# Kernel tuning notes

Hardware: AMD Instinct MI355X
Metric: run time of the kernel (lower is better)

## Reference

```python
import jax, jax.numpy as jnp
import numpy as np

IN_DIM, HID_DIM, OUT_DIM = 1024, 2048, 1024
DEG1, DEG2 = 8, 8
BATCH = 16384


def cheby_kan_layer(x, coeffs):
    """x: [b, i]; coeffs: [i, o, d+1] -> [b, o].
    Per-feature min-max normalize over batch to [-1,1], Chebyshev recurrence, contract."""
    degree = coeffs.shape[-1] - 1
    mn = jnp.min(x, axis=0, keepdims=True)
    mx = jnp.max(x, axis=0, keepdims=True)
    x = 2.0 * (x - mn) / (mx - mn) - 1.0
    Ts = [jnp.ones_like(x)]
    if degree > 0:
        Ts.append(x)
    for _ in range(2, degree + 1):
        Ts.append(2.0 * x * Ts[-1] - Ts[-2])
    cheby = jnp.stack(Ts, axis=-1)  # [b, i, d+1]
    return jnp.einsum('bid,iod->bo', cheby, coeffs)


def setup_inputs() -> dict:
    key = jax.random.key(0)
    k1, k2, k3 = jax.random.split(key, 3)
    x = jax.random.normal(k1, (BATCH, IN_DIM), dtype=jnp.float32)
    # kaiming-uniform-ish init for coeffs
    b1 = float(np.sqrt(6.0 / IN_DIM))
    b2 = float(np.sqrt(6.0 / HID_DIM))
    coeffs1 = jax.random.uniform(k2, (IN_DIM, HID_DIM, DEG1 + 1), dtype=jnp.float32, minval=-b1, maxval=b1)
    coeffs2 = jax.random.uniform(k3, (HID_DIM, OUT_DIM, DEG2 + 1), dtype=jnp.float32, minval=-b2, maxval=b2)
    return {"x": x, "coeffs1": coeffs1, "coeffs2": coeffs2}


def reference(x, coeffs1, coeffs2):
    h = cheby_kan_layer(x, coeffs1)
    y = cheby_kan_layer(h, coeffs2)
    return y
```

## Files before the change

kernel.cpp:

```cpp
#include <hip/hip_runtime.h>
#include <hip/hip_bf16.h>
#include <stdint.h>


constexpr int BATCH   = 16384;
constexpr int IN_DIM  = 1024;
constexpr int HID_DIM = 2048;
constexpr int OUT_DIM = 1024;
#define DP1 9

using bf16_t = __hip_bfloat16;

typedef __attribute__((ext_vector_type(4))) float f32x4;
typedef __attribute__((ext_vector_type(8))) short s16x8;
typedef __attribute__((ext_vector_type(16))) float f32x16;
typedef __attribute__((ext_vector_type(16))) __bf16 bf16x16;

static __device__ __forceinline__ unsigned int f2bf_u(float f) {
  union { __hip_bfloat16 h; unsigned short u; } cv;
  cv.h = __float2bfloat16(f);
  return (unsigned int)cv.u;
}

template <typename T>
__global__ void kan_minmax_partial(const T* __restrict__ x, int rows, int cols,
                                   float* __restrict__ mnp, float* __restrict__ mxp) {
  const int c  = blockIdx.x * 64 + (threadIdx.x & 63);
  const int rg = threadIdx.x >> 6;
  const int P  = gridDim.y;
  const int chunk = rows / P;
  const int r0 = blockIdx.y * chunk;
  float mn = 1e30f, mx = -1e30f;
  for (int r = r0 + rg; r < r0 + chunk; r += 4) {
    float v = (float)x[(size_t)r * cols + c];
    mn = fminf(mn, v); mx = fmaxf(mx, v);
  }
  __shared__ float smn[256], smx[256];
  smn[threadIdx.x] = mn; smx[threadIdx.x] = mx;
  __syncthreads();
  if (rg == 0) {
    int t = threadIdx.x;
    mn = fminf(fminf(smn[t], smn[t + 64]), fminf(smn[t + 128], smn[t + 192]));
    mx = fmaxf(fmaxf(smx[t], smx[t + 64]), fmaxf(smx[t + 128], smx[t + 192]));
    mnp[(size_t)blockIdx.y * cols + c] = mn;
    mxp[(size_t)blockIdx.y * cols + c] = mx;
  }
}

__global__ void kan_minmax_finalize(const float* __restrict__ mnp, const float* __restrict__ mxp,
                                    int cols, int P, float* __restrict__ s, float* __restrict__ t) {
  int c = blockIdx.x * blockDim.x + threadIdx.x;
  if (c >= cols) return;
  float mn = 1e30f, mx = -1e30f;
  for (int p = 0; p < P; ++p) {
    mn = fminf(mn, mnp[(size_t)p * cols + c]);
    mx = fmaxf(mx, mxp[(size_t)p * cols + c]);
  }
  float inv = 2.0f / (mx - mn);
  s[c] = inv;
  t[c] = -mn * inv - 1.0f;
}

__global__ void kan_repack(const float* __restrict__ coeffs, int I, int O,
                           bf16_t* __restrict__ Bp, float* __restrict__ biasp) {
  const int NIB = I / 32;
  const int ib = blockIdx.x % NIB;
  const int ntile = blockIdx.x / NIB;
  const size_t slab0 = (size_t)(ntile * NIB + ib) * 8 * 8192;
  __shared__ float sb[1024];
  for (int c = threadIdx.x; c < 1024; c += 256) {
    const int l16  = c & 15;
    const int quad = (c >> 4) & 3;
    const int ng   = c >> 6;
    const int o = ntile * 256 + ng * 16 + l16;
    const int ibase = ib * 32 + quad * 8;
    float v[8][9];
#pragma unroll
    for (int q = 0; q < 8; ++q) {
      const float* rp = coeffs + ((size_t)(ibase + q) * O + o) * DP1;
#pragma unroll
      for (int d = 0; d < 9; ++d) v[q][d] = rp[d];
    }
    float bsum = 0.f;
#pragma unroll
    for (int q = 0; q < 8; ++q) bsum += v[q][0];
    sb[c] = bsum;
#pragma unroll
    for (int d = 1; d < 9; ++d) {
      unsigned int pk[4];
#pragma unroll
      for (int q = 0; q < 4; ++q)
        pk[q] = f2bf_u(v[2 * q][d]) | (f2bf_u(v[2 * q + 1][d]) << 16);
      *reinterpret_cast<uint4*>(reinterpret_cast<char*>(Bp) +
          (slab0 + (size_t)(d - 1) * 8192 + (size_t)c * 8) * 2) =
          make_uint4(pk[0], pk[1], pk[2], pk[3]);
    }
  }
  __syncthreads();
  {
    const int t = threadIdx.x;
    const int ng = t >> 4, l16 = t & 15;
    const float s = sb[ng * 64 + l16] + sb[ng * 64 + 16 + l16] +
                    sb[ng * 64 + 32 + l16] + sb[ng * 64 + 48 + l16];
    biasp[(size_t)ib * O + ntile * 256 + t] = s;
  }
}

__global__ void kan_bias_finalize(const float* __restrict__ biasp, int NIB, int O,
                                  float* __restrict__ bias) {
  const int o = blockIdx.x * blockDim.x + threadIdx.x;
  if (o >= O) return;
  float s = 0.f;
  for (int p = 0; p < NIB; ++p) s += biasp[(size_t)p * O + o];
  bias[o] = s;
}

template <typename AT, typename OT>
__launch_bounds__(256, 2)
__global__ void kan_cheby_gemm(const AT* __restrict__ X, const bf16_t* __restrict__ Bp,
                               const float* __restrict__ sc, const float* __restrict__ tc,
                               const float* __restrict__ bias,
                               OT* __restrict__ out, int I, int N) {
  __shared__ __align__(16) short Als[2][4096];
  __shared__ __align__(16) short Bls[2][8192];
  __shared__ __align__(16) float scl[2048];
  __shared__ __align__(16) float tcl[2048];

  const int m0   = blockIdx.x * 128;
  const int tid  = threadIdx.x;
  const int lane = tid & 63;
  const int wave = tid >> 6;
  const int wr   = wave >> 1;
  const int wc   = wave & 1;
  const int wm4  = wr * 4;
  const int wn16 = wc * 8;
  const int quad = lane >> 4;
  const int l16  = lane & 15;

  const int ma = tid & 127;
  const int hf = tid >> 7;

  const int NIB = I / 32;
  const int nstage = NIB * 8;
  const size_t slab_base = (size_t)blockIdx.y * NIB * 8 * 8192;

  auto dma_b = [&](int ss) {
    const char* g = reinterpret_cast<const char*>(Bp + slab_base + (size_t)ss * 8192) +
                    wave * 4096 + lane * 16;
    char* l = reinterpret_cast<char*>(&Bls[ss & 1][0]) + wave * 4096;
#pragma unroll
    for (int t = 0; t < 4; ++t)
      __builtin_amdgcn_global_load_lds(
          (const __attribute__((address_space(1))) void*)(g + t * 1024),
          (__attribute__((address_space(3))) void*)(l + t * 1024), 16, 0, 0);
  };

  uint4 rq[4];
  auto load_raw = [&](int ibx) {
    const char* xp = reinterpret_cast<const char*>(
        X + (size_t)(m0 + ma) * I + ibx * 32 + hf * 16);
    if constexpr (sizeof(AT) == 4) {
      rq[0] = *reinterpret_cast<const uint4*>(xp +  0);
      rq[1] = *reinterpret_cast<const uint4*>(xp + 16);
      rq[2] = *reinterpret_cast<const uint4*>(xp + 32);
      rq[3] = *reinterpret_cast<const uint4*>(xp + 48);
    } else {
      rq[0] = *reinterpret_cast<const uint4*>(xp +  0);
      rq[1] = *reinterpret_cast<const uint4*>(xp + 16);
    }
  };

  f32x16 xv, Tm1, Tm2;
#pragma unroll
  for (int j = 0; j < 16; ++j) { xv[j] = 0.f; Tm1[j] = 0.f; Tm2[j] = 0.f; }

  auto unpack_norm = [&](int ibx) {
    const int fbase = ibx * 32 + hf * 16;
    float rv[16];
    const unsigned int* w = reinterpret_cast<const unsigned int*>(rq);
    if constexpr (sizeof(AT) == 4) {
#pragma unroll
      for (int j = 0; j < 16; ++j) rv[j] = __uint_as_float(w[j]);
    } else {
#pragma unroll
      for (int q = 0; q < 8; ++q) {
        rv[2 * q + 0] = __uint_as_float(w[q] << 16);
        rv[2 * q + 1] = __uint_as_float(w[q] & 0xffff0000u);
      }
    }
    const float4* sp = reinterpret_cast<const float4*>(&scl[fbase]);
    const float4* tp = reinterpret_cast<const float4*>(&tcl[fbase]);
#pragma unroll
    for (int v = 0; v < 4; ++v) {
      float4 s4 = sp[v], t4 = tp[v];
      xv[4 * v + 0] = fmaf(rv[4 * v + 0], s4.x, t4.x);
      xv[4 * v + 1] = fmaf(rv[4 * v + 1], s4.y, t4.y);
      xv[4 * v + 2] = fmaf(rv[4 * v + 2], s4.z, t4.z);
      xv[4 * v + 3] = fmaf(rv[4 * v + 3], s4.w, t4.w);
    }
  };

  auto write_a = [&](int buf, const f32x16& tv) {
    union { bf16x16 v; uint4 q[2]; } u;
    u.v = __builtin_convertvector(tv, bf16x16);
    char* b = reinterpret_cast<char*>(&Als[buf][0]) +
              (ma >> 4) * 1024 + hf * 512 + (ma & 15) * 16;
    *reinterpret_cast<uint4*>(b)       = u.q[0];
    *reinterpret_cast<uint4*>(b + 256) = u.q[1];
  };

  f32x4 acc[4][8] = {};

  for (int k = tid; k < I; k += 256) { scl[k] = sc[k]; tcl[k] = tc[k]; }
  load_raw(0);
  dma_b(0);
  __syncthreads();
  unpack_norm(0);
  write_a(0, xv);
  Tm1 = xv;
#pragma unroll
  for (int j = 0; j < 16; ++j) Tm2[j] = 1.0f;
  if (NIB > 1) load_raw(1);
  __syncthreads();

  for (int s = 0; s < nstage; ++s) {
    if (s + 1 < nstage) dma_b(s + 1);

    const char* Ab = reinterpret_cast<const char*>(&Als[s & 1][0]) + lane * 16;
    const char* Bb = reinterpret_cast<const char*>(&Bls[s & 1][0]) + lane * 16;
    s16x8 fa[4], fb[8];
#pragma unroll
    for (int mt = 0; mt < 4; ++mt)
      fa[mt] = *reinterpret_cast<const s16x8*>(Ab + (wm4 + mt) * 1024);
#pragma unroll
    for (int nt = 0; nt < 8; ++nt)
      fb[nt] = *reinterpret_cast<const s16x8*>(Bb + (wn16 + nt) * 1024);

    if (s + 1 < nstage) {
      const int t = s + 1;
      f32x16 tv;
      if ((t & 7) == 0) {
        const int ibn = t >> 3;
        unpack_norm(ibn);
        if (ibn + 1 < NIB) load_raw(ibn + 1);
        tv = Tm1 = xv;
#pragma unroll
        for (int j = 0; j < 16; ++j) Tm2[j] = 1.0f;
      } else {
        tv = 2.0f * xv * Tm1 - Tm2;
        Tm2 = Tm1; Tm1 = tv;
      }
      write_a(t & 1, tv);
    }

#pragma unroll
    for (int mt = 0; mt < 4; ++mt)
#pragma unroll
      for (int nt = 0; nt < 8; ++nt)
        acc[mt][nt] = __builtin_amdgcn_mfma_f32_16x16x32_bf16(
            fa[mt], fb[nt], acc[mt][nt], 0, 0, 0);

    __syncthreads();
  }

  const int n0 = blockIdx.y * 256;
  float bv[8];
#pragma unroll
  for (int nt = 0; nt < 8; ++nt)
    bv[nt] = bias[n0 + wc * 128 + nt * 16 + l16];
#pragma unroll
  for (int mt = 0; mt < 4; ++mt) {
#pragma unroll
    for (int nt = 0; nt < 8; ++nt) {
      const int n = n0 + wc * 128 + nt * 16 + l16;
#pragma unroll
      for (int r = 0; r < 4; ++r) {
        const int m = m0 + wr * 64 + mt * 16 + quad * 4 + r;
        float v = acc[mt][nt][r] + bv[nt];
        if constexpr (sizeof(OT) == 4)
          out[(size_t)m * N + n] = v;
        else
          out[(size_t)m * N + n] = __float2bfloat16(v);
      }
    }
  }
}

extern "C" void kernel_launch(void* const* d_in, const int* in_sizes, int n_in,
                              void* d_out, int out_size, void* d_ws, size_t ws_size,
                              hipStream_t stream) {
  const float* x  = (const float*)d_in[0];
  const float* c1 = (const float*)d_in[1];
  const float* c2 = (const float*)d_in[2];
  float* out = (float*)d_out;

  char* ws = (char*)d_ws;
  size_t off = 0;
  auto take = [&](size_t n) -> char* {
    char* p = ws + off;
    off += (n + 255) & ~(size_t)255;
    return p;
  };
  bf16_t* Bp1 = (bf16_t*)take((size_t)HID_DIM * IN_DIM  * 8 * 2);
  bf16_t* Bp2 = (bf16_t*)take((size_t)OUT_DIM * HID_DIM * 8 * 2);
  bf16_t* h   = (bf16_t*)take((size_t)BATCH * HID_DIM * 2);
  float* s1  = (float*)take(IN_DIM  * 4);
  float* t1  = (float*)take(IN_DIM  * 4);
  float* s2  = (float*)take(HID_DIM * 4);
  float* t2  = (float*)take(HID_DIM * 4);
  float* b1  = (float*)take(HID_DIM * 4);
  float* b2  = (float*)take(OUT_DIM * 4);
  float* bp1 = (float*)take((size_t)(IN_DIM / 32)  * HID_DIM * 4);
  float* bp2 = (float*)take((size_t)(HID_DIM / 32) * OUT_DIM * 4);
  float* mnp = (float*)take((size_t)16 * HID_DIM * 4);
  float* mxp = (float*)take((size_t)16 * HID_DIM * 4);

  kan_minmax_partial<float><<<dim3(IN_DIM / 64, 16), 256, 0, stream>>>(x, BATCH, IN_DIM, mnp, mxp);
  kan_minmax_finalize<<<dim3(IN_DIM / 256), 256, 0, stream>>>(mnp, mxp, IN_DIM, 16, s1, t1);
  kan_repack<<<dim3((HID_DIM / 256) * (IN_DIM / 32)), 256, 0, stream>>>(c1, IN_DIM, HID_DIM, Bp1, bp1);
  kan_bias_finalize<<<dim3(HID_DIM / 256), 256, 0, stream>>>(bp1, IN_DIM / 32, HID_DIM, b1);
  kan_repack<<<dim3((OUT_DIM / 256) * (HID_DIM / 32)), 256, 0, stream>>>(c2, HID_DIM, OUT_DIM, Bp2, bp2);
  kan_bias_finalize<<<dim3(OUT_DIM / 256), 256, 0, stream>>>(bp2, HID_DIM / 32, OUT_DIM, b2);
  kan_cheby_gemm<float, bf16_t><<<dim3(BATCH / 128, HID_DIM / 256), 256, 0, stream>>>(
      x, Bp1, s1, t1, b1, h, IN_DIM, HID_DIM);

  kan_minmax_partial<bf16_t><<<dim3(HID_DIM / 64, 16), 256, 0, stream>>>(h, BATCH, HID_DIM, mnp, mxp);
  kan_minmax_finalize<<<dim3(HID_DIM / 256), 256, 0, stream>>>(mnp, mxp, HID_DIM, 16, s2, t2);
  kan_cheby_gemm<bf16_t, float><<<dim3(BATCH / 128, OUT_DIM / 256), 256, 0, stream>>>(
      h, Bp2, s2, t2, b2, out, HID_DIM, OUT_DIM);
}
```

Measured before the change: 1.913 ms.

## Halve GEMM M-tile to 64 rows and raise occupancy to three blocks

The fused Chebyshev GEMM tile shrinks from 128x256 to 64x256. Each wave now covers all 64 rows and a 64-column slice, so it holds half the accumulators. The scale/shift LDS tables are dropped in favour of direct global loads, and launch bounds allow 3 blocks per CU to increase occupancy and latency hiding. In exchange, each 256-column B tile is reused across half as many rows, doubling B traffic from L2 per FLOP and lowering MFMA work per LDS read.

```diff
diff --git a/kernel.cpp b/kernel.cpp
--- a/kernel.cpp
+++ b/kernel.cpp
@@ -13,8 +13,8 @@
 
 typedef __attribute__((ext_vector_type(4))) float f32x4;
 typedef __attribute__((ext_vector_type(8))) short s16x8;
-typedef __attribute__((ext_vector_type(16))) float f32x16;
-typedef __attribute__((ext_vector_type(16))) __bf16 bf16x16;
+typedef __attribute__((ext_vector_type(8))) float f32x8;
+typedef __attribute__((ext_vector_type(8))) __bf16 bf16x8;
 
 static __device__ __forceinline__ unsigned int f2bf_u(float f) {
   union { __hip_bfloat16 h; unsigned short u; } cv;
@@ -116,29 +116,23 @@
 }
 
 template <typename AT, typename OT>
-__launch_bounds__(256, 2)
+__launch_bounds__(256, 3)
 __global__ void kan_cheby_gemm(const AT* __restrict__ X, const bf16_t* __restrict__ Bp,
                                const float* __restrict__ sc, const float* __restrict__ tc,
                                const float* __restrict__ bias,
                                OT* __restrict__ out, int I, int N) {
-  __shared__ __align__(16) short Als[2][4096];
+  __shared__ __align__(16) short Als[2][2048];
   __shared__ __align__(16) short Bls[2][8192];
-  __shared__ __align__(16) float scl[2048];
-  __shared__ __align__(16) float tcl[2048];
-
-  const int m0   = blockIdx.x * 128;
+
+  const int m0   = blockIdx.x * 64;
   const int tid  = threadIdx.x;
   const int lane = tid & 63;
   const int wave = tid >> 6;
-  const int wr   = wave >> 1;
-  const int wc   = wave & 1;
-  const int wm4  = wr * 4;
-  const int wn16 = wc * 8;
   const int quad = lane >> 4;
   const int l16  = lane & 15;
 
-  const int ma = tid & 127;
-  const int hf = tid >> 7;
+  const int ma = tid & 63;
+  const int hf = tid >> 6;
 
   const int NIB = I / 32;
   const int nstage = NIB * 8;
@@ -155,43 +149,40 @@
           (__attribute__((address_space(3))) void*)(l + t * 1024), 16, 0, 0);
   };
 
-  uint4 rq[4];
+  uint4 rq[2];
   auto load_raw = [&](int ibx) {
     const char* xp = reinterpret_cast<const char*>(
-        X + (size_t)(m0 + ma) * I + ibx * 32 + hf * 16);
+        X + (size_t)(m0 + ma) * I + ibx * 32 + hf * 8);
     if constexpr (sizeof(AT) == 4) {
       rq[0] = *reinterpret_cast<const uint4*>(xp +  0);
       rq[1] = *reinterpret_cast<const uint4*>(xp + 16);
-      rq[2] = *reinterpret_cast<const uint4*>(xp + 32);
-      rq[3] = *reinterpret_cast<const uint4*>(xp + 48);
     } else {
-      rq[0] = *reinterpret_cast<const uint4*>(xp +  0);
-      rq[1] = *reinterpret_cast<const uint4*>(xp + 16);
-    }
-  };
-
-  f32x16 xv, Tm1, Tm2;
-#pragma unroll
-  for (int j = 0; j < 16; ++j) { xv[j] = 0.f; Tm1[j] = 0.f; Tm2[j] = 0.f; }
+      rq[0] = *reinterpret_cast<const uint4*>(xp);
+    }
+  };
+
+  f32x8 xv, Tm1, Tm2;
+#pragma unroll
+  for (int j = 0; j < 8; ++j) { xv[j] = 0.f; Tm1[j] = 0.f; Tm2[j] = 0.f; }
 
   auto unpack_norm = [&](int ibx) {
-    const int fbase = ibx * 32 + hf * 16;
-    float rv[16];
+    const int fbase = ibx * 32 + hf * 8;
+    float rv[8];
     const unsigned int* w = reinterpret_cast<const unsigned int*>(rq);
     if constexpr (sizeof(AT) == 4) {
 #pragma unroll
-      for (int j = 0; j < 16; ++j) rv[j] = __uint_as_float(w[j]);
+      for (int j = 0; j < 8; ++j) rv[j] = __uint_as_float(w[j]);
     } else {
 #pragma unroll
-      for (int q = 0; q < 8; ++q) {
+      for (int q = 0; q < 4; ++q) {
         rv[2 * q + 0] = __uint_as_float(w[q] << 16);
         rv[2 * q + 1] = __uint_as_float(w[q] & 0xffff0000u);
       }
     }
-    const float4* sp = reinterpret_cast<const float4*>(&scl[fbase]);
-    const float4* tp = reinterpret_cast<const float4*>(&tcl[fbase]);
-#pragma unroll
-    for (int v = 0; v < 4; ++v) {
+    const float4* sp = reinterpret_cast<const float4*>(sc + fbase);
+    const float4* tp = reinterpret_cast<const float4*>(tc + fbase);
+#pragma unroll
+    for (int v = 0; v < 2; ++v) {
       float4 s4 = sp[v], t4 = tp[v];
       xv[4 * v + 0] = fmaf(rv[4 * v + 0], s4.x, t4.x);
       xv[4 * v + 1] = fmaf(rv[4 * v + 1], s4.y, t4.y);
@@ -200,26 +191,23 @@
     }
   };
 
-  auto write_a = [&](int buf, const f32x16& tv) {
-    union { bf16x16 v; uint4 q[2]; } u;
-    u.v = __builtin_convertvector(tv, bf16x16);
+  auto write_a = [&](int buf, const f32x8& tv) {
+    union { bf16x8 v; uint4 q; } u;
+    u.v = __builtin_convertvector(tv, bf16x8);
     char* b = reinterpret_cast<char*>(&Als[buf][0]) +
-              (ma >> 4) * 1024 + hf * 512 + (ma & 15) * 16;
-    *reinterpret_cast<uint4*>(b)       = u.q[0];
-    *reinterpret_cast<uint4*>(b + 256) = u.q[1];
-  };
-
-  f32x4 acc[4][8] = {};
-
-  for (int k = tid; k < I; k += 256) { scl[k] = sc[k]; tcl[k] = tc[k]; }
+              (ma >> 4) * 1024 + hf * 256 + (ma & 15) * 16;
+    *reinterpret_cast<uint4*>(b) = u.q;
+  };
+
+  f32x4 acc[4][4] = {};
+
   load_raw(0);
   dma_b(0);
-  __syncthreads();
   unpack_norm(0);
   write_a(0, xv);
   Tm1 = xv;
 #pragma unroll
-  for (int j = 0; j < 16; ++j) Tm2[j] = 1.0f;
+  for (int j = 0; j < 8; ++j) Tm2[j] = 1.0f;
   if (NIB > 1) load_raw(1);
   __syncthreads();
 
@@ -228,24 +216,24 @@
 
     const char* Ab = reinterpret_cast<const char*>(&Als[s & 1][0]) + lane * 16;
     const char* Bb = reinterpret_cast<const char*>(&Bls[s & 1][0]) + lane * 16;
-    s16x8 fa[4], fb[8];
+    s16x8 fa[4], fb[4];
 #pragma unroll
     for (int mt = 0; mt < 4; ++mt)
-      fa[mt] = *reinterpret_cast<const s16x8*>(Ab + (wm4 + mt) * 1024);
-#pragma unroll
-    for (int nt = 0; nt < 8; ++nt)
-      fb[nt] = *reinterpret_cast<const s16x8*>(Bb + (wn16 + nt) * 1024);
+      fa[mt] = *reinterpret_cast<const s16x8*>(Ab + mt * 1024);
+#pragma unroll
+    for (int nt = 0; nt < 4; ++nt)
+      fb[nt] = *reinterpret_cast<const s16x8*>(Bb + (wave * 4 + nt) * 1024);
 
     if (s + 1 < nstage) {
       const int t = s + 1;
-      f32x16 tv;
+      f32x8 tv;
       if ((t & 7) == 0) {
         const int ibn = t >> 3;
         unpack_norm(ibn);
         if (ibn + 1 < NIB) load_raw(ibn + 1);
         tv = Tm1 = xv;
 #pragma unroll
-        for (int j = 0; j < 16; ++j) Tm2[j] = 1.0f;
+        for (int j = 0; j < 8; ++j) Tm2[j] = 1.0f;
       } else {
         tv = 2.0f * xv * Tm1 - Tm2;
         Tm2 = Tm1; Tm1 = tv;
@@ -256,7 +244,7 @@
 #pragma unroll
     for (int mt = 0; mt < 4; ++mt)
 #pragma unroll
-      for (int nt = 0; nt < 8; ++nt)
+      for (int nt = 0; nt < 4; ++nt)
         acc[mt][nt] = __builtin_amdgcn_mfma_f32_16x16x32_bf16(
             fa[mt], fb[nt], acc[mt][nt], 0, 0, 0);
 
@@ -264,18 +252,18 @@
   }
 
   const int n0 = blockIdx.y * 256;
-  float bv[8];
-#pragma unroll
-  for (int nt = 0; nt < 8; ++nt)
-    bv[nt] = bias[n0 + wc * 128 + nt * 16 + l16];
+  float bv[4];
+#pragma unroll
+  for (int nt = 0; nt < 4; ++nt)
+    bv[nt] = bias[n0 + wave * 64 + nt * 16 + l16];
 #pragma unroll
   for (int mt = 0; mt < 4; ++mt) {
 #pragma unroll
-    for (int nt = 0; nt < 8; ++nt) {
-      const int n = n0 + wc * 128 + nt * 16 + l16;
+    for (int nt = 0; nt < 4; ++nt) {
+      const int n = n0 + wave * 64 + nt * 16 + l16;
 #pragma unroll
       for (int r = 0; r < 4; ++r) {
-        const int m = m0 + wr * 64 + mt * 16 + quad * 4 + r;
+        const int m = m0 + mt * 16 + quad * 4 + r;
         float v = acc[mt][nt][r] + bv[nt];
         if constexpr (sizeof(OT) == 4)
           out[(size_t)m * N + n] = v;
@@ -321,11 +309,11 @@
   kan_bias_finalize<<<dim3(HID_DIM / 256), 256, 0, stream>>>(bp1, IN_DIM / 32, HID_DIM, b1);
   kan_repack<<<dim3((OUT_DIM / 256) * (HID_DIM / 32)), 256, 0, stream>>>(c2, HID_DIM, OUT_DIM, Bp2, bp2);
   kan_bias_finalize<<<dim3(OUT_DIM / 256), 256, 0, stream>>>(bp2, HID_DIM / 32, OUT_DIM, b2);
-  kan_cheby_gemm<float, bf16_t><<<dim3(BATCH / 128, HID_DIM / 256), 256, 0, stream>>>(
+  kan_cheby_gemm<float, bf16_t><<<dim3(BATCH / 64, HID_DIM / 256), 256, 0, stream>>>(
       x, Bp1, s1, t1, b1, h, IN_DIM, HID_DIM);
 
   kan_minmax_partial<bf16_t><<<dim3(HID_DIM / 64, 16), 256, 0, stream>>>(h, BATCH, HID_DIM, mnp, mxp);
   kan_minmax_finalize<<<dim3(HID_DIM / 256), 256, 0, stream>>>(mnp, mxp, HID_DIM, 16, s2, t2);
-  kan_cheby_gemm<bf16_t, float><<<dim3(BATCH / 128, OUT_DIM / 256), 256, 0, stream>>>(
+  kan_cheby_gemm<bf16_t, float><<<dim3(BATCH / 64, OUT_DIM / 256), 256, 0, stream>>>(
       h, Bp2, s2, t2, b2, out, HID_DIM, OUT_DIM);
 }
```

Result: slower. 2.001 ms (+4.6%).
